# Kernel optimization log

Hardware: AMD Instinct MI355X
Metric: run time of the kernel (lower is better)

The kernel has to match this reference:

```python
import jax, jax.numpy as jnp
import numpy as np

B, C, H, W = 32, 256, 128, 128
VIEWS, K = 9, 3
PAD = (K - 1) // 2


def setup_inputs() -> dict:
    key = jax.random.key(0)
    k1, k2, k3, k4, k5 = jax.random.split(key, 5)
    x = jax.random.normal(k1, (B, C, H, W), dtype=jnp.float32)
    kernels_u = jax.random.normal(k2, (VIEWS, 1, C, K, K), dtype=jnp.float32) * 0.01
    kernels_v = jax.random.normal(k3, (VIEWS, 1, C, K, K), dtype=jnp.float32) * 0.01
    u_indices = jax.random.randint(k4, (B,), 0, VIEWS)
    v_indices = jax.random.randint(k5, (B,), 0, VIEWS)
    return {"x": x, "kernels_u": kernels_u, "kernels_v": kernels_v,
            "u_indices": u_indices, "v_indices": v_indices}


def reference(x, kernels_u, kernels_v, u_indices, v_indices):
    b, c, h, w = x.shape
    # Gather per-sample kernels: [B,1,C,3,3] each
    k_u = kernels_u[u_indices]
    k_v = kernels_v[v_indices]
    # [B,2,C,3,3] -> grouped-conv weights [2B, C, 3, 3]
    weights = jnp.concatenate([k_u, k_v], axis=1).reshape(b * 2, c, K, K)
    # Reflect-pad then treat batch as groups: lhs [1, B*C, H+2p, W+2p]
    x_pad = jnp.pad(x, ((0, 0), (0, 0), (PAD, PAD), (PAD, PAD)), mode="reflect")
    lhs = x_pad.reshape(1, b * c, h + 2 * PAD, w + 2 * PAD)
    out = jax.lax.conv_general_dilated(
        lhs, weights,
        window_strides=(1, 1), padding="VALID",
        dimension_numbers=("NCHW", "OIHW", "NCHW"),
        feature_group_count=b,
    )  # [1, 2B, H, W]
    return out.reshape(b, 2, h, w)
```

## Files before the change

kernel.cpp:

```cpp
#include <hip/hip_runtime.h>

constexpr int Bc = 32;
constexpr int Cc = 256;
constexpr int Hc = 128;
constexpr int Wc = 128;
constexpr int HWc = Hc * Wc;
constexpr int CHUNKS = 2;
constexpr int CPC = Cc / CHUNKS;
constexpr int ROWS = 16;
constexpr int TILES = Hc / ROWS;

__global__ __launch_bounds__(512) void zero_out_kernel(float4* __restrict__ out4) {
    int i = blockIdx.x * 512 + threadIdx.x;
    out4[i] = make_float4(0.f, 0.f, 0.f, 0.f);
}

__global__ __launch_bounds__(512, 4) void modbank_kernel(
    const float* __restrict__ x,
    const float* __restrict__ ku,
    const float* __restrict__ kv,
    const int*   __restrict__ ui,
    const int*   __restrict__ vi,
    float* __restrict__ out)
{
    const int tile  = blockIdx.x;
    const int b     = blockIdx.y;
    const int chunk = blockIdx.z;
    const int c0    = chunk * CPC;
    const int tid   = threadIdx.x;

    const int w4 = tid & 31;
    const int r  = tid >> 5;
    const int h  = tile * ROWS + r;
    const int hm = (h == 0)      ? 1      : h - 1;
    const int hp = (h == Hc - 1) ? Hc - 2 : h + 1;

    const float* pm = x + ((size_t)(b * Cc + c0) * Hc + hm) * Wc + w4 * 4;
    const float* p0 = x + ((size_t)(b * Cc + c0) * Hc + h ) * Wc + w4 * 4;
    const float* pp = x + ((size_t)(b * Cc + c0) * Hc + hp) * Wc + w4 * 4;

    const int uview = ui[b];
    const int vview = vi[b];
    const float* wub = ku + ((size_t)uview * Cc + c0) * 9;
    const float* wvb = kv + ((size_t)vview * Cc + c0) * 9;

    const float eL = (w4 == 0)  ? 1.f : 0.f;
    const float eR = (w4 == 31) ? 1.f : 0.f;

    float  aum1 = 0.f, au4 = 0.f, avm1 = 0.f, av4 = 0.f;
    float4 au = make_float4(0.f, 0.f, 0.f, 0.f);
    float4 av = make_float4(0.f, 0.f, 0.f, 0.f);

    auto rowc = [](const float4& v, float tL, float tR,
                   float ka, float kb, float kc,
                   float& am1, float4& a, float& a4) {
        am1 = fmaf(kc, v.x, am1);
        a.x = fmaf(kb, v.x, fmaf(kc, v.y, fmaf(ka, tL, a.x)));
        a.y = fmaf(ka, v.x, fmaf(kb, v.y, fmaf(kc, v.z, a.y)));
        a.z = fmaf(ka, v.y, fmaf(kb, v.z, fmaf(kc, v.w, a.z)));
        a.w = fmaf(ka, v.z, fmaf(kb, v.w, fmaf(kc, tR, a.w)));
        a4  = fmaf(ka, v.w, a4);
    };

    #pragma unroll 2
    for (int ci = 0; ci < CPC; ++ci) {
        const float4 vm = *(const float4*)pm; pm += HWc;
        const float4 v0 = *(const float4*)p0; p0 += HWc;
        const float4 vp = *(const float4*)pp; pp += HWc;
        const float* wu = wub + ci * 9;
        const float* wv = wvb + ci * 9;

        const float tLm = eL * vm.y, tRm = eR * vm.z;
        const float tL0 = eL * v0.y, tR0 = eR * v0.z;
        const float tLp = eL * vp.y, tRp = eR * vp.z;

        rowc(vm, tLm, tRm, wu[0], wu[1], wu[2], aum1, au, au4);
        rowc(v0, tL0, tR0, wu[3], wu[4], wu[5], aum1, au, au4);
        rowc(vp, tLp, tRp, wu[6], wu[7], wu[8], aum1, au, au4);
        rowc(vm, tLm, tRm, wv[0], wv[1], wv[2], avm1, av, av4);
        rowc(v0, tL0, tR0, wv[3], wv[4], wv[5], avm1, av, av4);
        rowc(vp, tLp, tRp, wv[6], wv[7], wv[8], avm1, av, av4);
    }

    float fLu = __shfl_up(au4, 1);    if (w4 == 0)  fLu = 0.f;
    float fLv = __shfl_up(av4, 1);    if (w4 == 0)  fLv = 0.f;
    float fRu = __shfl_down(aum1, 1); if (w4 == 31) fRu = 0.f;
    float fRv = __shfl_down(avm1, 1); if (w4 == 31) fRv = 0.f;
    au.x += fLu; au.w += fRu;
    av.x += fLv; av.w += fRv;

    float* ou = out + ((size_t)(b * 2 + 0) * Hc + h) * Wc + w4 * 4;
    float* ov = out + ((size_t)(b * 2 + 1) * Hc + h) * Wc + w4 * 4;
    atomicAdd(ou + 0, au.x); atomicAdd(ou + 1, au.y);
    atomicAdd(ou + 2, au.z); atomicAdd(ou + 3, au.w);
    atomicAdd(ov + 0, av.x); atomicAdd(ov + 1, av.y);
    atomicAdd(ov + 2, av.z); atomicAdd(ov + 3, av.w);
}

extern "C" void kernel_launch(void* const* d_in, const int* in_sizes, int n_in,
                              void* d_out, int out_size, void* d_ws, size_t ws_size,
                              hipStream_t stream) {
    const float* x  = (const float*)d_in[0];
    const float* ku = (const float*)d_in[1];
    const float* kv = (const float*)d_in[2];
    const int*   ui = (const int*)d_in[3];
    const int*   vi = (const int*)d_in[4];
    float* out = (float*)d_out;

    zero_out_kernel<<<512, 512, 0, stream>>>((float4*)out);

    dim3 grid(TILES, Bc, CHUNKS);
    modbank_kernel<<<grid, 512, 0, stream>>>(x, ku, kv, ui, vi, out);
}
```

Baseline: 726.2 us.

## Drop channel split and atomics; write outputs directly with one block per tile

Removes the two-way channel chunking so each block accumulates all 256 channels and stores its results with plain float4 writes. This eliminates the separate zero-fill kernel and the per-element atomic adds into the output. In exchange, the grid is halved and each thread runs a longer serial loop. That reduces the number of waves available to hide memory latency in a bandwidth-bound kernel.

Measured after the change: 760.4 us. 1.05x slower.

```diff
diff --git a/kernel.cpp b/kernel.cpp
--- a/kernel.cpp
+++ b/kernel.cpp
@@ -5,17 +5,10 @@
 constexpr int Hc = 128;
 constexpr int Wc = 128;
 constexpr int HWc = Hc * Wc;
-constexpr int CHUNKS = 2;
-constexpr int CPC = Cc / CHUNKS;
 constexpr int ROWS = 16;
 constexpr int TILES = Hc / ROWS;
 
-__global__ __launch_bounds__(512) void zero_out_kernel(float4* __restrict__ out4) {
-    int i = blockIdx.x * 512 + threadIdx.x;
-    out4[i] = make_float4(0.f, 0.f, 0.f, 0.f);
-}
-
-__global__ __launch_bounds__(512, 4) void modbank_kernel(
+__global__ __launch_bounds__(512, 2) void modbank_kernel(
     const float* __restrict__ x,
     const float* __restrict__ ku,
     const float* __restrict__ kv,
@@ -25,8 +18,6 @@
 {
     const int tile  = blockIdx.x;
     const int b     = blockIdx.y;
-    const int chunk = blockIdx.z;
-    const int c0    = chunk * CPC;
     const int tid   = threadIdx.x;
 
     const int w4 = tid & 31;
@@ -35,14 +26,14 @@
     const int hm = (h == 0)      ? 1      : h - 1;
     const int hp = (h == Hc - 1) ? Hc - 2 : h + 1;
 
-    const float* pm = x + ((size_t)(b * Cc + c0) * Hc + hm) * Wc + w4 * 4;
-    const float* p0 = x + ((size_t)(b * Cc + c0) * Hc + h ) * Wc + w4 * 4;
-    const float* pp = x + ((size_t)(b * Cc + c0) * Hc + hp) * Wc + w4 * 4;
+    const float* pm = x + ((size_t)b * Cc * Hc + hm) * Wc + w4 * 4;
+    const float* p0 = x + ((size_t)b * Cc * Hc + h ) * Wc + w4 * 4;
+    const float* pp = x + ((size_t)b * Cc * Hc + hp) * Wc + w4 * 4;
 
     const int uview = ui[b];
     const int vview = vi[b];
-    const float* wub = ku + ((size_t)uview * Cc + c0) * 9;
-    const float* wvb = kv + ((size_t)vview * Cc + c0) * 9;
+    const float* wub = ku + (size_t)uview * Cc * 9;
+    const float* wvb = kv + (size_t)vview * Cc * 9;
 
     const float eL = (w4 == 0)  ? 1.f : 0.f;
     const float eR = (w4 == 31) ? 1.f : 0.f;
@@ -63,7 +54,7 @@
     };
 
     #pragma unroll 2
-    for (int ci = 0; ci < CPC; ++ci) {
+    for (int ci = 0; ci < Cc; ++ci) {
         const float4 vm = *(const float4*)pm; pm += HWc;
         const float4 v0 = *(const float4*)p0; p0 += HWc;
         const float4 vp = *(const float4*)pp; pp += HWc;
@@ -89,12 +80,10 @@
     au.x += fLu; au.w += fRu;
     av.x += fLv; av.w += fRv;
 
-    float* ou = out + ((size_t)(b * 2 + 0) * Hc + h) * Wc + w4 * 4;
-    float* ov = out + ((size_t)(b * 2 + 1) * Hc + h) * Wc + w4 * 4;
-    atomicAdd(ou + 0, au.x); atomicAdd(ou + 1, au.y);
-    atomicAdd(ou + 2, au.z); atomicAdd(ou + 3, au.w);
-    atomicAdd(ov + 0, av.x); atomicAdd(ov + 1, av.y);
-    atomicAdd(ov + 2, av.z); atomicAdd(ov + 3, av.w);
+    float4* ou = (float4*)(out + ((size_t)(b * 2 + 0) * Hc + h) * Wc) + w4;
+    float4* ov = (float4*)(out + ((size_t)(b * 2 + 1) * Hc + h) * Wc) + w4;
+    *ou = au;
+    *ov = av;
 }
 
 extern "C" void kernel_launch(void* const* d_in, const int* in_sizes, int n_in,
@@ -107,8 +96,6 @@
     const int*   vi = (const int*)d_in[4];
     float* out = (float*)d_out;
 
-    zero_out_kernel<<<512, 512, 0, stream>>>((float4*)out);
-
-    dim3 grid(TILES, Bc, CHUNKS);
+    dim3 grid(TILES, Bc);
     modbank_kernel<<<grid, 512, 0, stream>>>(x, ku, kv, ui, vi, out);
 }
```
